# Optimization experiments

Hardware: AMD Instinct MI355X
Metric: run time of the kernel (lower is better)

## Reference

```python
import jax, jax.numpy as jnp
import numpy as np

D = 768
N_HEADS = 12
HEAD_DIM = 64
INNER = N_HEADS * HEAD_DIM
SCALE = HEAD_DIM ** -0.5
EPS = 1e-5


def setup_inputs() -> dict:
    key = jax.random.key(0)
    ks = jax.random.split(key, 7)
    s = 0.02
    return {
        "x": jax.random.normal(ks[0], (2, 2048, D), dtype=jnp.float32),
        "Wq": jax.random.normal(ks[1], (D, INNER), dtype=jnp.float32) * s,
        "Wk": jax.random.normal(ks[2], (D, INNER), dtype=jnp.float32) * s,
        "Wv": jax.random.normal(ks[3], (D, INNER), dtype=jnp.float32) * s,
        "Wo": jax.random.normal(ks[4], (INNER, D), dtype=jnp.float32) * s,
        "bo": jnp.zeros((D,), dtype=jnp.float32),
        "gamma": jnp.ones((D,), dtype=jnp.float32),
        "beta": jnp.zeros((D,), dtype=jnp.float32),
    }


def _layernorm(x, gamma, beta):
    mu = jnp.mean(x, axis=-1, keepdims=True)
    var = jnp.var(x, axis=-1, keepdims=True)
    return (x - mu) * jax.lax.rsqrt(var + EPS) * gamma + beta


def reference(x, Wq, Wk, Wv, Wo, bo, gamma, beta):
    b, n, _ = x.shape
    h = _layernorm(x, gamma, beta)
    # project and split heads: [b, n, inner] -> [b, h, n, d]
    def split(t):
        return t.reshape(b, n, N_HEADS, HEAD_DIM).transpose(0, 2, 1, 3)
    Q = split(h @ Wq)
    K = split(h @ Wk)
    V = split(h @ Wv)
    # NOTE: module applies softmax first, THEN multiplies probs by scale
    attn = jnp.einsum('bhid,bhjd->bhij', Q, K)
    attn = jax.nn.softmax(attn, axis=-1) * SCALE
    vals = jnp.einsum('bhij,bhjd->bhid', attn, V)
    vals = vals.transpose(0, 2, 1, 3).reshape(b, n, INNER)
    out = vals @ Wo + bo
    return x + out
```

## Files before the change

### kernel.cpp

```cpp
#include <hip/hip_runtime.h>
#include <stdint.h>

typedef __bf16 bf16;
typedef __bf16 bf16x8 __attribute__((ext_vector_type(8)));
typedef float  f32x4  __attribute__((ext_vector_type(4)));
typedef unsigned short u16x4 __attribute__((ext_vector_type(4)));
typedef unsigned int   u32x4v __attribute__((ext_vector_type(4)));

#define SEQ   2048
#define DM    768
#define NH    12
#define HD    64
#define ATT_SCALE 0.125f
#define LOG2E 1.44269504f
#define LN_EPS 1e-5f

__device__ __forceinline__ void gload16(const void* g, void* l) {
  __builtin_amdgcn_global_load_lds((const __attribute__((address_space(1))) void*)g,
                                   (__attribute__((address_space(3))) void*)l,
                                   16, 0, 0);
}

__global__ __launch_bounds__(256) void prep_kernel(
    const float* __restrict__ x, const float* __restrict__ gamma,
    const float* __restrict__ beta, bf16* __restrict__ h,
    const float* __restrict__ Wq, const float* __restrict__ Wk,
    const float* __restrict__ Wv, const float* __restrict__ Wo,
    bf16* __restrict__ Wqkvt, bf16* __restrict__ Wot)
{
  __shared__ float smem[32*33];
  int bid = blockIdx.x, t = threadIdx.x;
  if (bid < 4096) {
    const float* xr = x + (size_t)bid*DM;
    float v0 = xr[t], v1 = xr[t+256], v2 = xr[t+512];
    float s = v0+v1+v2;
    float q = v0*v0+v1*v1+v2*v2;
    #pragma unroll
    for (int m=32;m>=1;m>>=1){ s += __shfl_xor(s,m,64); q += __shfl_xor(q,m,64); }
    float* rs = smem; float* rq = smem+8;
    int w = t>>6;
    if ((t&63)==0){ rs[w]=s; rq[w]=q; }
    __syncthreads();
    float S = rs[0]+rs[1]+rs[2]+rs[3];
    float Q = rq[0]+rq[1]+rq[2]+rq[3];
    float mean = S*(1.0f/DM);
    float var  = Q*(1.0f/DM) - mean*mean;
    float rstd = rsqrtf(var + LN_EPS);
    bf16* hr = h + (size_t)bid*DM;
    hr[t]     = (bf16)((v0-mean)*rstd*gamma[t]     + beta[t]);
    hr[t+256] = (bf16)((v1-mean)*rstd*gamma[t+256] + beta[t+256]);
    hr[t+512] = (bf16)((v2-mean)*rstd*gamma[t+512] + beta[t+512]);
  } else {
    int tb = bid - 4096;
    int z = tb/576, rem = tb%576;
    int r0 = (rem/24)*32, c0 = (rem%24)*32;
    int tx = t&31, ty = t>>5;
    float (*tile)[33] = (float(*)[33])smem;
    const float* src = (z==0)?Wq:(z==1)?Wk:(z==2)?Wv:Wo;
    #pragma unroll
    for (int i=ty;i<32;i+=8) tile[i][tx] = src[(size_t)(r0+i)*DM + c0+tx];
    __syncthreads();
    bf16* dst = (z<3) ? (Wqkvt + (size_t)z*DM*DM) : Wot;
    #pragma unroll
    for (int i=ty;i<32;i+=8) dst[(size_t)(c0+i)*DM + r0+tx] = (bf16)tile[tx][i];
  }
}

template<int BM, int BN, int WM, int WN, int EPI>
__global__ __launch_bounds__(256) void gemm_bt(
    const bf16* __restrict__ A, const bf16* __restrict__ Bt, int K,
    bf16* __restrict__ qk, bf16* __restrict__ vt,
    float* __restrict__ out, const float* __restrict__ bo, const float* __restrict__ xres)
{
  constexpr int MF = BM/(WM*16);
  constexpr int NF = BN/(WN*16);
  constexpr int GL = BM/64 + BN/64;
  __shared__ bf16 As[3][BM][32];
  __shared__ bf16 Bs[3][BN][32];
  int tid = threadIdx.x, w = tid>>6, la = tid&63;
  int bn = blockIdx.x, bm = blockIdx.y;
  int wm = w / WN, wn = w % WN;
  int g = la>>4, li = la&15;
  int sr = la>>2, sc = (la&3)*8;
  f32x4 acc[MF][NF] = {};
  const int KT = K/32;

  auto stage = [&](int kt, int bb) {
    int k0 = kt*32;
    #pragma unroll
    for (int i=0;i<BM/64;i++){ int r0 = i*64 + w*16;
      gload16(A + ((size_t)(bm*BM + r0 + sr))*K + k0 + sc, &As[bb][r0][0]); }
    #pragma unroll
    for (int i=0;i<BN/64;i++){ int r0 = i*64 + w*16;
      gload16(Bt + ((size_t)(bn*BN + r0 + sr))*K + k0 + sc, &Bs[bb][r0][0]); }
  };

  stage(0,0); stage(1,1);
  asm volatile("s_waitcnt vmcnt(%0)" :: "n"(GL) : "memory");
  __builtin_amdgcn_s_barrier();
  __builtin_amdgcn_sched_barrier(0);

  for (int kt=0; kt<KT; ++kt) {
    int bb = kt%3;
    if (kt+2 < KT) stage(kt+2, (kt+2)%3);
    bf16x8 af[MF], bfr[NF];
    #pragma unroll
    for (int i=0;i<MF;i++) af[i]  = *(const bf16x8*)&As[bb][wm*(BM/WM)+i*16+li][g*8];
    #pragma unroll
    for (int j=0;j<NF;j++) bfr[j] = *(const bf16x8*)&Bs[bb][wn*(BN/WN)+j*16+li][g*8];
    __builtin_amdgcn_s_setprio(1);
    #pragma unroll
    for (int i=0;i<MF;i++)
      #pragma unroll
      for (int j=0;j<NF;j++)
        acc[i][j] = __builtin_amdgcn_mfma_f32_16x16x32_bf16(af[i], bfr[j], acc[i][j], 0,0,0);
    __builtin_amdgcn_s_setprio(0);
    if (kt+1 < KT) {
      if (kt+2 < KT) asm volatile("s_waitcnt vmcnt(%0)" :: "n"(GL) : "memory");
      else           asm volatile("s_waitcnt vmcnt(0)" ::: "memory");
      __builtin_amdgcn_s_barrier();
      __builtin_amdgcn_sched_barrier(0);
    }
  }

  #pragma unroll
  for (int i=0;i<MF;i++){
    int row0 = bm*BM + wm*(BM/WM) + i*16 + g*4;
    #pragma unroll
    for (int j=0;j<NF;j++){
      int col = bn*BN + wn*(BN/WN) + j*16 + li;
      if (EPI==0){
        if (col < 1536) {
          float qs = (col < 768) ? LOG2E : 1.0f;
          #pragma unroll
          for (int r=0;r<4;r++) qk[(size_t)(row0+r)*1536 + col] = (bf16)(acc[i][j][r]*qs);
        } else {
          int cv = col - 1536; int hh = cv>>6, dd = cv&63;
          int b_ = row0>>11,  n0 = row0&2047;
          u16x4 u;
          #pragma unroll
          for (int r=0;r<4;r++){ bf16 bv = (bf16)acc[i][j][r];
            u[r] = __builtin_bit_cast(unsigned short, bv); }
          *reinterpret_cast<u16x4*>(vt + ((size_t)((b_*NH+hh)*HD+dd))*SEQ + n0) = u;
        }
      } else {
        float bb2 = bo[col];
        #pragma unroll
        for (int r=0;r<4;r++){ size_t idx = (size_t)(row0+r)*DM + col;
          out[idx] = acc[i][j][r] + bb2 + xres[idx]; }
      }
    }
  }
}

__global__ __launch_bounds__(128) void attn_kernel(
    const bf16* __restrict__ QK, const bf16* __restrict__ Vt,
    bf16* __restrict__ Opart, float* __restrict__ lpart)
{
  __shared__ bf16 Ks[2][64][64];
  __shared__ bf16 Vs[2][64][64];
  int tid=threadIdx.x, w=tid>>6, la=tid&63;
  int id = blockIdx.x;
  int xcd = id & 7, idx = id >> 3;
  int bh  = xcd*3 + idx/64;
  int rem = idx & 63;
  int qt  = rem >> 1;
  int kvh = rem & 1;
  int b = bh/NH, hh = bh%NH;
  int g=la>>4, li=la&15;
  int lr=la>>3;
  int lx=li&7;
  int lcs=((la&7)^lr)*8;
  size_t qrow0=(size_t)b*SEQ + qt*64;
  int kv0 = kvh*1024;

  bf16x8 qf[2][2];
  #pragma unroll
  for (int qh=0;qh<2;qh++){
    const bf16* qp = QK + (qrow0 + w*32 + qh*16 + li)*1536 + hh*64;
    qf[0][qh] = *(const bf16x8*)(qp + g*8);
    qf[1][qh] = *(const bf16x8*)(qp + 32 + g*8);
  }

  bf16x8 onef;
  {
    unsigned int one2 = 0x3F803F80u;
    u32x4v oc = {one2, one2, one2, one2};
    onef = __builtin_bit_cast(bf16x8, oc);
  }

  const bf16* Kbase = QK + (size_t)b*SEQ*1536 + 768 + hh*64;
  const bf16* Vbase = Vt + (size_t)(b*NH+hh)*HD*SEQ;

  auto stage = [&](int tt, int bb) {
    int j0 = kv0 + tt*64;
    #pragma unroll
    for (int i=0;i<4;i++){ int c=i*2+w;
      gload16(Kbase + (size_t)(j0 + c*8 + lr)*1536 + lcs, &Ks[bb][c*8][0]);
      gload16(Vbase + (size_t)(c*8 + lr)*SEQ + j0 + lcs,  &Vs[bb][c*8][0]); }
  };

  stage(0,0);
  asm volatile("s_waitcnt vmcnt(0)" ::: "memory");
  __builtin_amdgcn_s_barrier();
  __builtin_amdgcn_sched_barrier(0);

  f32x4 o[2][4] = {};
  f32x4 ol[2] = {};

  for (int t=0;t<16;t++){
    int bb = t&1;
    if (t+1 < 16) stage(t+1, bb^1);
    f32x4 s[2][4] = {};
    #pragma unroll
    for (int kk=0;kk<2;kk++){
      bf16x8 kf[4];
      #pragma unroll
      for (int nf=0;nf<4;nf++){
        int row = nf*16+li;
        kf[nf] = *(const bf16x8*)((const char*)&Ks[bb][0][0] + row*128 + (((kk*4+g)^lx)<<4));
      }
      __builtin_amdgcn_s_setprio(1);
      #pragma unroll
      for (int nf=0;nf<4;nf++){
        s[0][nf] = __builtin_amdgcn_mfma_f32_16x16x32_bf16(kf[nf], qf[kk][0], s[0][nf], 0,0,0);
        s[1][nf] = __builtin_amdgcn_mfma_f32_16x16x32_bf16(kf[nf], qf[kk][1], s[1][nf], 0,0,0);
      }
      __builtin_amdgcn_s_setprio(0);
    }
    bf16x8 pa[2][2];
    #pragma unroll
    for (int qh=0;qh<2;qh++){
      float p[4][4];
      #pragma unroll
      for (int nf=0;nf<4;nf++)
        #pragma unroll
        for (int r=0;r<4;r++)
          p[nf][r] = __builtin_amdgcn_exp2f(s[qh][nf][r]);
      #pragma unroll
      for (int ks=0;ks<2;ks++){
        unsigned int c00,c01,c10,c11;
        asm("v_cvt_pk_bf16_f32 %0, %1, %2" : "=v"(c00) : "v"(p[2*ks  ][0]), "v"(p[2*ks  ][1]));
        asm("v_cvt_pk_bf16_f32 %0, %1, %2" : "=v"(c01) : "v"(p[2*ks  ][2]), "v"(p[2*ks  ][3]));
        asm("v_cvt_pk_bf16_f32 %0, %1, %2" : "=v"(c10) : "v"(p[2*ks+1][0]), "v"(p[2*ks+1][1]));
        asm("v_cvt_pk_bf16_f32 %0, %1, %2" : "=v"(c11) : "v"(p[2*ks+1][2]), "v"(p[2*ks+1][3]));
        asm("v_permlane32_swap_b32 %0, %1" : "+v"(c00), "+v"(c10));
        asm("v_permlane32_swap_b32 %0, %1" : "+v"(c01), "+v"(c11));
        asm("v_permlane16_swap_b32 %0, %1" : "+v"(c00), "+v"(c10));
        asm("v_permlane16_swap_b32 %0, %1" : "+v"(c01), "+v"(c11));
        u32x4v cc = {c00, c01, c10, c11};
        pa[qh][ks] = __builtin_bit_cast(bf16x8, cc);
      }
    }
    #pragma unroll
    for (int ks=0;ks<2;ks++){
      bf16x8 vb[4];
      #pragma unroll
      for (int df=0;df<4;df++){
        int row = df*16+li;
        vb[df] = *(const bf16x8*)((const char*)&Vs[bb][0][0] + row*128 + (((ks*4+g)^lx)<<4));
      }
      __builtin_amdgcn_s_setprio(1);
      #pragma unroll
      for (int qh=0;qh<2;qh++){
        #pragma unroll
        for (int df=0;df<4;df++)
          o[qh][df] = __builtin_amdgcn_mfma_f32_16x16x32_bf16(vb[df], pa[qh][ks], o[qh][df], 0,0,0);
        ol[qh] = __builtin_amdgcn_mfma_f32_16x16x32_bf16(onef, pa[qh][ks], ol[qh], 0,0,0);
      }
      __builtin_amdgcn_s_setprio(0);
    }
    if (t+1 < 16) {
      asm volatile("s_waitcnt vmcnt(0)" ::: "memory");
      __builtin_amdgcn_s_barrier();
      __builtin_amdgcn_sched_barrier(0);
    }
  }
  bf16* ob = Opart + (size_t)kvh*4096*DM;
  #pragma unroll
  for (int qh=0;qh<2;qh++){
    size_t row = qrow0 + w*32 + qh*16 + li;
    #pragma unroll
    for (int df=0;df<4;df++){
      u16x4 u;
      #pragma unroll
      for (int r=0;r<4;r++){
        bf16 bv = (bf16)o[qh][df][r];
        u[r] = __builtin_bit_cast(unsigned short, bv);
      }
      *reinterpret_cast<u16x4*>(ob + row*DM + hh*64 + df*16 + g*4) = u;
    }
    if (g==0) lpart[(size_t)kvh*24*SEQ + (size_t)bh*SEQ + qt*64 + w*32 + qh*16 + li] = ol[qh][0];
  }
}

__global__ __launch_bounds__(256) void reduce_kernel(
    const bf16* __restrict__ Op, const float* __restrict__ lp, bf16* __restrict__ vals)
{
  int gid = blockIdx.x*256 + threadIdx.x;
  int r = gid/96, cv = gid - r*96;
  int c0 = cv*8;
  int b = r>>11, q = r&2047, h = c0>>6;
  size_t li = (size_t)(b*NH + h)*SEQ + q;
  float l = lp[li] + lp[(size_t)24*SEQ + li];
  float fac = ATT_SCALE / l;
  bf16x8 a = *(const bf16x8*)(Op + (size_t)r*DM + c0);
  bf16x8 bb = *(const bf16x8*)(Op + (size_t)4096*DM + (size_t)r*DM + c0);
  bf16x8 o;
  #pragma unroll
  for (int i=0;i<8;i++) o[i] = (bf16)(((float)a[i] + (float)bb[i]) * fac);
  *(bf16x8*)(vals + (size_t)r*DM + c0) = o;
}

extern "C" void kernel_launch(void* const* d_in, const int* in_sizes, int n_in,
                              void* d_out, int out_size, void* d_ws, size_t ws_size,
                              hipStream_t stream)
{
  const float* x     = (const float*)d_in[0];
  const float* Wq    = (const float*)d_in[1];
  const float* Wk    = (const float*)d_in[2];
  const float* Wv    = (const float*)d_in[3];
  const float* Wo    = (const float*)d_in[4];
  const float* bo    = (const float*)d_in[5];
  const float* gamma = (const float*)d_in[6];
  const float* beta  = (const float*)d_in[7];
  float* out = (float*)d_out;
  char* ws = (char*)d_ws;

  bf16* h     = (bf16*)(ws + 0);
  bf16* vals  = (bf16*)(ws + 0);
  bf16* Wqkvt = (bf16*)(ws + 6291456);
  bf16* Wot   = (bf16*)(ws + 9830400);
  bf16* QKb   = (bf16*)(ws + 11010048);
  bf16* Vt    = (bf16*)(ws + 23592960);
  bf16*  Opart = (bf16*)d_out;
  float* lpart = (float*)(ws + 6291456);
  (void)ws_size; (void)in_sizes; (void)n_in; (void)out_size;

  prep_kernel<<<dim3(6400), dim3(256), 0, stream>>>(
      x, gamma, beta, h, Wq, Wk, Wv, Wo, Wqkvt, Wot);
  gemm_bt<128,128,2,2,0><<<dim3(18,32), dim3(256), 0, stream>>>(
      h, Wqkvt, DM, QKb, Vt, nullptr, nullptr, nullptr);
  attn_kernel<<<dim3(1536), dim3(128), 0, stream>>>(QKb, Vt, Opart, lpart);
  reduce_kernel<<<dim3(1536), dim3(256), 0, stream>>>(Opart, lpart, vals);
  gemm_bt<64,64,2,2,1><<<dim3(12,64), dim3(256), 0, stream>>>(
      vals, Wot, DM, nullptr, nullptr, out, bo, x);
}
```

Baseline: 116.1 us.

## Use four waves of 16 query rows in attention and sum row totals on VALU

The attention block grows from 2 waves covering 32 query rows each to 4 waves covering 16 rows each, so per-wave accumulators and Q fragments shrink and each wave issues half the K/V staging loads. The row-sum of probabilities is now accumulated with VALU adds plus cross-lane shuffles instead of an extra MFMA against a ones vector. This aims for more parallelism per block and less MFMA work and register pressure. In exchange each K/V tile in LDS is reused by more waves, with more barrier participants per tile, and the VALU load per wave rises.

Result: faster. 107.2 us (-7.7%).

```diff
diff --git a/kernel.cpp b/kernel.cpp
--- a/kernel.cpp
+++ b/kernel.cpp
@@ -153,7 +153,7 @@
   }
 }
 
-__global__ __launch_bounds__(128) void attn_kernel(
+__global__ __launch_bounds__(256) void attn_kernel(
     const bf16* __restrict__ QK, const bf16* __restrict__ Vt,
     bf16* __restrict__ Opart, float* __restrict__ lpart)
 {
@@ -174,19 +174,11 @@
   size_t qrow0=(size_t)b*SEQ + qt*64;
   int kv0 = kvh*1024;
 
-  bf16x8 qf[2][2];
-  #pragma unroll
-  for (int qh=0;qh<2;qh++){
-    const bf16* qp = QK + (qrow0 + w*32 + qh*16 + li)*1536 + hh*64;
-    qf[0][qh] = *(const bf16x8*)(qp + g*8);
-    qf[1][qh] = *(const bf16x8*)(qp + 32 + g*8);
-  }
-
-  bf16x8 onef;
+  bf16x8 qf[2];
   {
-    unsigned int one2 = 0x3F803F80u;
-    u32x4v oc = {one2, one2, one2, one2};
-    onef = __builtin_bit_cast(bf16x8, oc);
+    const bf16* qp = QK + (qrow0 + w*16 + li)*1536 + hh*64;
+    qf[0] = *(const bf16x8*)(qp + g*8);
+    qf[1] = *(const bf16x8*)(qp + 32 + g*8);
   }
 
   const bf16* Kbase = QK + (size_t)b*SEQ*1536 + 768 + hh*64;
@@ -195,7 +187,7 @@
   auto stage = [&](int tt, int bb) {
     int j0 = kv0 + tt*64;
     #pragma unroll
-    for (int i=0;i<4;i++){ int c=i*2+w;
+    for (int i=0;i<2;i++){ int c=i*4+w;
       gload16(Kbase + (size_t)(j0 + c*8 + lr)*1536 + lcs, &Ks[bb][c*8][0]);
       gload16(Vbase + (size_t)(c*8 + lr)*SEQ + j0 + lcs,  &Vs[bb][c*8][0]); }
   };
@@ -205,13 +197,13 @@
   __builtin_amdgcn_s_barrier();
   __builtin_amdgcn_sched_barrier(0);
 
-  f32x4 o[2][4] = {};
-  f32x4 ol[2] = {};
+  f32x4 o[4] = {};
+  float lp[4] = {0.f,0.f,0.f,0.f};
 
   for (int t=0;t<16;t++){
     int bb = t&1;
     if (t+1 < 16) stage(t+1, bb^1);
-    f32x4 s[2][4] = {};
+    f32x4 s[4] = {};
     #pragma unroll
     for (int kk=0;kk<2;kk++){
       bf16x8 kf[4];
@@ -222,35 +214,33 @@
       }
       __builtin_amdgcn_s_setprio(1);
       #pragma unroll
-      for (int nf=0;nf<4;nf++){
-        s[0][nf] = __builtin_amdgcn_mfma_f32_16x16x32_bf16(kf[nf], qf[kk][0], s[0][nf], 0,0,0);
-        s[1][nf] = __builtin_amdgcn_mfma_f32_16x16x32_bf16(kf[nf], qf[kk][1], s[1][nf], 0,0,0);
+      for (int nf=0;nf<4;nf++)
+        s[nf] = __builtin_amdgcn_mfma_f32_16x16x32_bf16(kf[nf], qf[kk], s[nf], 0,0,0);
+      __builtin_amdgcn_s_setprio(0);
+    }
+    float p[4][4];
+    #pragma unroll
+    for (int nf=0;nf<4;nf++){
+      #pragma unroll
+      for (int r=0;r<4;r++){
+        p[nf][r] = __builtin_amdgcn_exp2f(s[nf][r]);
+        lp[nf] += p[nf][r];
       }
-      __builtin_amdgcn_s_setprio(0);
-    }
-    bf16x8 pa[2][2];
-    #pragma unroll
-    for (int qh=0;qh<2;qh++){
-      float p[4][4];
-      #pragma unroll
-      for (int nf=0;nf<4;nf++)
-        #pragma unroll
-        for (int r=0;r<4;r++)
-          p[nf][r] = __builtin_amdgcn_exp2f(s[qh][nf][r]);
-      #pragma unroll
-      for (int ks=0;ks<2;ks++){
-        unsigned int c00,c01,c10,c11;
-        asm("v_cvt_pk_bf16_f32 %0, %1, %2" : "=v"(c00) : "v"(p[2*ks  ][0]), "v"(p[2*ks  ][1]));
-        asm("v_cvt_pk_bf16_f32 %0, %1, %2" : "=v"(c01) : "v"(p[2*ks  ][2]), "v"(p[2*ks  ][3]));
-        asm("v_cvt_pk_bf16_f32 %0, %1, %2" : "=v"(c10) : "v"(p[2*ks+1][0]), "v"(p[2*ks+1][1]));
-        asm("v_cvt_pk_bf16_f32 %0, %1, %2" : "=v"(c11) : "v"(p[2*ks+1][2]), "v"(p[2*ks+1][3]));
-        asm("v_permlane32_swap_b32 %0, %1" : "+v"(c00), "+v"(c10));
-        asm("v_permlane32_swap_b32 %0, %1" : "+v"(c01), "+v"(c11));
-        asm("v_permlane16_swap_b32 %0, %1" : "+v"(c00), "+v"(c10));
-        asm("v_permlane16_swap_b32 %0, %1" : "+v"(c01), "+v"(c11));
-        u32x4v cc = {c00, c01, c10, c11};
-        pa[qh][ks] = __builtin_bit_cast(bf16x8, cc);
-      }
+    }
+    bf16x8 pa[2];
+    #pragma unroll
+    for (int ks=0;ks<2;ks++){
+      unsigned int c00,c01,c10,c11;
+      asm("v_cvt_pk_bf16_f32 %0, %1, %2" : "=v"(c00) : "v"(p[2*ks  ][0]), "v"(p[2*ks  ][1]));
+      asm("v_cvt_pk_bf16_f32 %0, %1, %2" : "=v"(c01) : "v"(p[2*ks  ][2]), "v"(p[2*ks  ][3]));
+      asm("v_cvt_pk_bf16_f32 %0, %1, %2" : "=v"(c10) : "v"(p[2*ks+1][0]), "v"(p[2*ks+1][1]));
+      asm("v_cvt_pk_bf16_f32 %0, %1, %2" : "=v"(c11) : "v"(p[2*ks+1][2]), "v"(p[2*ks+1][3]));
+      asm("v_permlane32_swap_b32 %0, %1" : "+v"(c00), "+v"(c10));
+      asm("v_permlane32_swap_b32 %0, %1" : "+v"(c01), "+v"(c11));
+      asm("v_permlane16_swap_b32 %0, %1" : "+v"(c00), "+v"(c10));
+      asm("v_permlane16_swap_b32 %0, %1" : "+v"(c01), "+v"(c11));
+      u32x4v cc = {c00, c01, c10, c11};
+      pa[ks] = __builtin_bit_cast(bf16x8, cc);
     }
     #pragma unroll
     for (int ks=0;ks<2;ks++){
@@ -262,12 +252,8 @@
       }
       __builtin_amdgcn_s_setprio(1);
       #pragma unroll
-      for (int qh=0;qh<2;qh++){
-        #pragma unroll
-        for (int df=0;df<4;df++)
-          o[qh][df] = __builtin_amdgcn_mfma_f32_16x16x32_bf16(vb[df], pa[qh][ks], o[qh][df], 0,0,0);
-        ol[qh] = __builtin_amdgcn_mfma_f32_16x16x32_bf16(onef, pa[qh][ks], ol[qh], 0,0,0);
-      }
+      for (int df=0;df<4;df++)
+        o[df] = __builtin_amdgcn_mfma_f32_16x16x32_bf16(vb[df], pa[ks], o[df], 0,0,0);
       __builtin_amdgcn_s_setprio(0);
     }
     if (t+1 < 16) {
@@ -276,22 +262,22 @@
       __builtin_amdgcn_sched_barrier(0);
     }
   }
+  float lsum = lp[0]+lp[1]+lp[2]+lp[3];
+  lsum += __shfl_xor(lsum, 16, 64);
+  lsum += __shfl_xor(lsum, 32, 64);
   bf16* ob = Opart + (size_t)kvh*4096*DM;
+  size_t row = qrow0 + w*16 + li;
   #pragma unroll
-  for (int qh=0;qh<2;qh++){
-    size_t row = qrow0 + w*32 + qh*16 + li;
-    #pragma unroll
-    for (int df=0;df<4;df++){
-      u16x4 u;
-      #pragma unroll
-      for (int r=0;r<4;r++){
-        bf16 bv = (bf16)o[qh][df][r];
-        u[r] = __builtin_bit_cast(unsigned short, bv);
-      }
-      *reinterpret_cast<u16x4*>(ob + row*DM + hh*64 + df*16 + g*4) = u;
-    }
-    if (g==0) lpart[(size_t)kvh*24*SEQ + (size_t)bh*SEQ + qt*64 + w*32 + qh*16 + li] = ol[qh][0];
-  }
+  for (int df=0;df<4;df++){
+    u16x4 u;
+    #pragma unroll
+    for (int r=0;r<4;r++){
+      bf16 bv = (bf16)o[df][r];
+      u[r] = __builtin_bit_cast(unsigned short, bv);
+    }
+    *reinterpret_cast<u16x4*>(ob + row*DM + hh*64 + df*16 + g*4) = u;
+  }
+  if (g==0) lpart[(size_t)kvh*24*SEQ + (size_t)bh*SEQ + qt*64 + w*16 + li] = lsum;
 }
 
 __global__ __launch_bounds__(256) void reduce_kernel(
@@ -341,7 +327,7 @@
       x, gamma, beta, h, Wq, Wk, Wv, Wo, Wqkvt, Wot);
   gemm_bt<128,128,2,2,0><<<dim3(18,32), dim3(256), 0, stream>>>(
       h, Wqkvt, DM, QKb, Vt, nullptr, nullptr, nullptr);
-  attn_kernel<<<dim3(1536), dim3(128), 0, stream>>>(QKb, Vt, Opart, lpart);
+  attn_kernel<<<dim3(1536), dim3(256), 0, stream>>>(QKb, Vt, Opart, lpart);
   reduce_kernel<<<dim3(1536), dim3(256), 0, stream>>>(Opart, lpart, vals);
   gemm_bt<64,64,2,2,1><<<dim3(12,64), dim3(256), 0, stream>>>(
       vals, Wot, DM, nullptr, nullptr, out, bo, x);
```
